# Kernel tuning notes

Hardware: AMD Instinct MI355X
Metric: run time of the kernel (lower is better)

The kernel has to match this reference:

```python
import jax, jax.numpy as jnp
import numpy as np

N_HEAD = 16

def setup_inputs() -> dict:
    key = jax.random.key(0)
    ks = jax.random.split(key, 5)
    B, S, D = 4, 2048, 1024
    return {
        "string": jax.random.normal(ks[0], (B, S, D), dtype=jnp.float32),
        "string_len": jax.random.randint(ks[1], (B,), 1, S + 1),
        "Wqkv": jax.random.normal(ks[2], (D, 3 * D), dtype=jnp.float32) * 0.02,
        "bqkv": jnp.zeros((3 * D,), dtype=jnp.float32),
        "Wo": jax.random.normal(ks[3], (D, D), dtype=jnp.float32) * 0.02,
        "bo": jnp.zeros((D,), dtype=jnp.float32),
    }


def reference(string, string_len, Wqkv, bqkv, Wo, bo):
    B, S, D = string.shape
    H = N_HEAD
    hd = D // H
    x = string @ Wqkv + bqkv                      # [B,S,3D]
    q, k, v = jnp.split(x, 3, axis=-1)
    # split heads -> [B,H,S,hd]
    q = q.reshape(B, S, H, hd).transpose(0, 2, 1, 3)
    k = k.reshape(B, S, H, hd).transpose(0, 2, 1, 3)
    v = v.reshape(B, S, H, hd).transpose(0, 2, 1, 3)
    w = jnp.einsum('bhqd,bhkd->bhqk', q, k) / jnp.sqrt(jnp.float32(hd))
    causal = jnp.tril(jnp.ones((S, S), dtype=bool))  # [S,S]
    w = jnp.where(causal[None, None], w, jnp.float32(-1e9))
    w = jax.nn.softmax(w, axis=-1)
    a = jnp.einsum('bhqk,bhkd->bhqd', w, v)       # [B,H,S,hd]
    a = a.transpose(0, 2, 1, 3).reshape(B, S, D)  # merge heads
    a = a @ Wo + bo
    return a, string_len
```

## Files before the change

kernel.cpp:

```cpp
#include <hip/hip_runtime.h>
#include <stdint.h>

typedef __attribute__((ext_vector_type(8))) short bf16x8;
typedef __attribute__((ext_vector_type(4))) float f32x4;
typedef __attribute__((ext_vector_type(16))) float f32x16;
typedef __attribute__((ext_vector_type(4))) unsigned short u16x4;

static constexpr int Bn = 4, Sn = 2048, Dn = 1024, Hn = 16, HD = 64;
static constexpr int Mrows = Bn * Sn;
static constexpr int D3 = 3 * Dn;

__device__ __forceinline__ unsigned short f2bf(float f) {
  unsigned int u = __float_as_uint(f);
  u += 0x7FFF + ((u >> 16) & 1);
  return (unsigned short)(u >> 16);
}

__device__ __forceinline__ void gload16(const void* gptr, void* lptr) {
  __builtin_amdgcn_global_load_lds(
      (__attribute__((address_space(1))) void*)gptr,
      (__attribute__((address_space(3))) void*)lptr, 16, 0, 0);
}

__device__ __forceinline__ int swz8(int r) { return (r ^ (r >> 3)) & 7; }

__device__ __forceinline__ float vexp2(float x) {
#if __has_builtin(__builtin_amdgcn_exp2f)
  return __builtin_amdgcn_exp2f(x);
#else
  return exp2f(x);
#endif
}

__device__ __forceinline__ unsigned cvtpk(float lo, float hi) {
  unsigned r;
  asm("v_cvt_pk_bf16_f32 %0, %1, %2" : "=v"(r) : "v"(lo), "v"(hi));
  return r;
}

__device__ __forceinline__ float lanepull(float v, int srclane) {
  return __int_as_float(__builtin_amdgcn_ds_bpermute(srclane * 4, __float_as_int(v)));
}

__global__ void cvt_f32_bf16(const float* __restrict__ in,
                             unsigned short* __restrict__ out, int n) {
  int i = (blockIdx.x * blockDim.x + threadIdx.x) * 4;
  if (i < n) {
    const float4 v = *(const float4*)(in + i);
    u16x4 o;
    o.x = f2bf(v.x); o.y = f2bf(v.y); o.z = f2bf(v.z); o.w = f2bf(v.w);
    *(u16x4*)(out + i) = o;
  }
}

__global__ void transpose_cvt(const float* __restrict__ W,
                              unsigned short* __restrict__ Wt, int K, int N) {
  __shared__ float tile[32][33];
  const int n0 = blockIdx.x * 32, k0 = blockIdx.y * 32;
  const int tx = threadIdx.x, ty = threadIdx.y;
  #pragma unroll
  for (int j = 0; j < 4; j++)
    tile[ty + 8 * j][tx] = W[(size_t)(k0 + ty + 8 * j) * N + n0 + tx];
  __syncthreads();
  #pragma unroll
  for (int j = 0; j < 4; j++)
    Wt[(size_t)(n0 + ty + 8 * j) * K + k0 + tx] = f2bf(tile[tx][ty + 8 * j]);
}

template<bool BF16_OUT>
__global__ __launch_bounds__(512, 1)
void gemm_bt2(const unsigned short* __restrict__ A,
              const unsigned short* __restrict__ Bt,
              const float* __restrict__ bias,
              void* __restrict__ Cout, int Nt, int Kt) {
  __shared__ __align__(128) unsigned char smem[98304];
  const int tid = threadIdx.x;
  const int w = tid >> 6, lane = tid & 63;
  const int wm = w >> 2, wn = w & 3;
  const int lrow = lane & 15, lk = lane >> 4;
  const long brow = (long)blockIdx.x * 128;
  const long bcol = (long)blockIdx.y * 256;

  const int srow = tid >> 3;
  const int sslot = tid & 7;

  auto stage = [&](int k0, unsigned char* buf) {
    unsigned char* Ab = buf;
    unsigned char* Bb = buf + 16384;
    #pragma unroll
    for (int i = 0; i < 2; i++) {
      const int r = srow + 64 * i;
      gload16(A + (size_t)(brow + r) * Kt + k0 + ((sslot ^ swz8(r)) * 8),
              Ab + w * 1024 + i * 8192);
    }
    #pragma unroll
    for (int i = 0; i < 4; i++) {
      const int r = srow + 64 * i;
      gload16(Bt + (size_t)(bcol + r) * Kt + k0 + ((sslot ^ swz8(r)) * 8),
              Bb + w * 1024 + i * 8192);
    }
  };

  f32x4 acc[4][4] = {};

  stage(0, smem);

  const int ntile = Kt >> 6;
  for (int t = 0; t < ntile; t++) {
    const int cur = t & 1;
    unsigned char* Ab = smem + cur * 49152;
    unsigned char* Bb = Ab + 16384;

    __builtin_amdgcn_s_barrier();
    if (t + 1 < ntile) {
      stage((t + 1) << 6, smem + (cur ^ 1) * 49152);
      asm volatile("s_waitcnt vmcnt(6)");
    } else {
      asm volatile("s_waitcnt vmcnt(0)");
    }
    __builtin_amdgcn_sched_barrier(0);
    __builtin_amdgcn_s_barrier();

    bf16x8 af[4][2], bfv[4][2];
    #pragma unroll
    for (int mt = 0; mt < 4; mt++) {
      const int r = wm * 64 + mt * 16 + lrow;
      #pragma unroll
      for (int kk = 0; kk < 2; kk++)
        af[mt][kk] = *(const bf16x8*)(Ab + r * 128 + (((kk * 4 + lk) ^ swz8(r)) * 16));
    }
    #pragma unroll
    for (int nt = 0; nt < 4; nt++) {
      const int r = wn * 64 + nt * 16 + lrow;
      #pragma unroll
      for (int kk = 0; kk < 2; kk++)
        bfv[nt][kk] = *(const bf16x8*)(Bb + r * 128 + (((kk * 4 + lk) ^ swz8(r)) * 16));
    }
    __builtin_amdgcn_s_setprio(1);
    #pragma unroll
    for (int mt = 0; mt < 4; mt++)
      #pragma unroll
      for (int nt = 0; nt < 4; nt++) {
        acc[mt][nt] = __builtin_amdgcn_mfma_f32_16x16x32_bf16(af[mt][0], bfv[nt][0], acc[mt][nt], 0, 0, 0);
        acc[mt][nt] = __builtin_amdgcn_mfma_f32_16x16x32_bf16(af[mt][1], bfv[nt][1], acc[mt][nt], 0, 0, 0);
      }
    __builtin_amdgcn_s_setprio(0);
  }

  #pragma unroll
  for (int nt = 0; nt < 4; nt++) {
    const long col = bcol + wn * 64 + nt * 16 + lrow;
    const float bv = bias[col];
    #pragma unroll
    for (int mt = 0; mt < 4; mt++) {
      #pragma unroll
      for (int rr = 0; rr < 4; rr++) {
        const long row = brow + wm * 64 + mt * 16 + lk * 4 + rr;
        const float v = acc[mt][nt][rr] + bv;
        if (BF16_OUT)
          ((unsigned short*)Cout)[row * Nt + col] = f2bf(v);
        else
          ((float*)Cout)[row * Nt + col] = v;
      }
    }
  }
}

__global__ __launch_bounds__(512, 2)
void attn_fwd2(const unsigned short* __restrict__ QKV,
               unsigned short* __restrict__ Out) {
  __shared__ __align__(128) unsigned char smem[65536];
  const int tid  = threadIdx.x;
  const int w    = tid >> 6;
  const int lane = tid & 63;
  const int li = lane & 31, hi = lane >> 5;
  const int bh = blockIdx.x;
  const int b  = bh >> 4, h = bh & 15;
  const int pb = blockIdx.y;
  const int qs = (w < 4) ? (63 - 4 * pb - w) : (4 * pb + (w - 4));
  const int wq = qs * 32;
  const int qrow = wq + li;

  bf16x8 qf[4];
  {
    const unsigned short* qp = QKV + (size_t)(b * Sn + qrow) * D3 + h * HD + hi * 8;
    #pragma unroll
    for (int ks = 0; ks < 4; ks++) qf[ks] = *(const bf16x8*)(qp + ks * 16);
  }

  f32x16 o0 = {}, o1 = {};
  float m = -3.0e38f, lsum = 0.f;
  const float cexp = 0.18033688011112042f;

  auto kstage = [&](int kb, unsigned char* Kb) {
    #pragma unroll
    for (int i = 0; i < 2; i++) {
      const int r    = w * 16 + i * 8 + (lane >> 3);
      const int slot = (lane & 7) ^ swz8(r);
      gload16(QKV + (size_t)(b * Sn + kb + r) * D3 + Dn + h * HD + slot * 8,
              Kb + w * 2048 + i * 1024);
    }
  };
  const int vkv8 = tid >> 3;
  const int vd0  = (tid & 7) * 8;
  auto vload = [&](int kb, int i) -> bf16x8 {
    return *(const bf16x8*)(QKV + (size_t)(b * Sn + kb + i * 64 + vkv8) * D3 + 2 * Dn + h * HD + vd0);
  };
  auto vwrite = [&](bf16x8 vv, int i, unsigned char* Vb) {
    const int kv = i * 64 + vkv8;
    #pragma unroll
    for (int j = 0; j < 8; j++) {
      const int d  = vd0 + j;
      const int vs = (d ^ (d >> 3)) & 15;
      *(unsigned short*)(Vb + d * 256 + (((kv >> 3) ^ vs) << 4) + (kv & 7) * 2) = (unsigned short)vv[j];
    }
  };

  auto substep = [&](int s, int kb, const unsigned char* Kb, const unsigned char* Vb) {
    f32x16 s0 = {}, s1 = {};
    const int r0 = s * 64 + li, r1 = s * 64 + 32 + li;
    __builtin_amdgcn_s_setprio(1);
    #pragma unroll
    for (int ks = 0; ks < 4; ks++) {
      const int slot = ks * 2 + hi;
      const bf16x8 k0 = *(const bf16x8*)(Kb + r0 * 128 + ((slot ^ swz8(r0)) * 16));
      const bf16x8 k1 = *(const bf16x8*)(Kb + r1 * 128 + ((slot ^ swz8(r1)) * 16));
      s0 = __builtin_amdgcn_mfma_f32_32x32x16_bf16(k0, qf[ks], s0, 0, 0, 0);
      s1 = __builtin_amdgcn_mfma_f32_32x32x16_bf16(k1, qf[ks], s1, 0, 0, 0);
    }
    __builtin_amdgcn_s_setprio(0);
    const int kbase = kb + s * 64;
    if (kbase + 63 > wq) {
      #pragma unroll
      for (int r = 0; r < 16; r++) {
        const int kvl = (r & 3) + 8 * (r >> 2) + 4 * hi;
        if (kbase + kvl > qrow)      s0[r] = -3.0e38f;
        if (kbase + 32 + kvl > qrow) s1[r] = -3.0e38f;
      }
    }
    float t8[8];
    #pragma unroll
    for (int r = 0; r < 8; r++)
      t8[r] = fmaxf(fmaxf(s0[r], s0[r + 8]), fmaxf(s1[r], s1[r + 8]));
    float tmax = fmaxf(fmaxf(fmaxf(t8[0], t8[1]), fmaxf(t8[2], t8[3])),
                       fmaxf(fmaxf(t8[4], t8[5]), fmaxf(t8[6], t8[7])));
    tmax = fmaxf(tmax, __shfl_xor(tmax, 32));
    if (__any(tmax > m + 44.0f)) {
      const float mn   = fmaxf(m, tmax);
      const float corr = vexp2((m - mn) * cexp);
      m = mn;
      lsum *= corr;
      #pragma unroll
      for (int r = 0; r < 16; r++) {
        const float cr = lanepull(corr, (r & 3) + 8 * (r >> 2) + 4 * hi);
        o0[r] *= cr; o1[r] *= cr;
      }
    }
    const float mc = m * cexp;
    f32x16 p0, p1;
    float psa = 0.f, psb = 0.f, psc = 0.f, psd = 0.f;
    #pragma unroll
    for (int r = 0; r < 16; r += 4) {
      p0[r] = vexp2(fmaf(s0[r], cexp, -mc));         psa += p0[r];
      p0[r + 1] = vexp2(fmaf(s0[r + 1], cexp, -mc)); psb += p0[r + 1];
      p0[r + 2] = vexp2(fmaf(s0[r + 2], cexp, -mc)); psc += p0[r + 2];
      p0[r + 3] = vexp2(fmaf(s0[r + 3], cexp, -mc)); psd += p0[r + 3];
    }
    #pragma unroll
    for (int r = 0; r < 16; r += 4) {
      p1[r] = vexp2(fmaf(s1[r], cexp, -mc));         psa += p1[r];
      p1[r + 1] = vexp2(fmaf(s1[r + 1], cexp, -mc)); psb += p1[r + 1];
      p1[r + 2] = vexp2(fmaf(s1[r + 2], cexp, -mc)); psc += p1[r + 2];
      p1[r + 3] = vexp2(fmaf(s1[r + 3], cexp, -mc)); psd += p1[r + 3];
    }
    lsum += (psa + psb) + (psc + psd);

    auto mk_pa = [&](const f32x16& pp, int base) -> bf16x8 {
      const unsigned a0 = cvtpk(pp[base + 0], pp[base + 1]);
      const unsigned a1 = cvtpk(pp[base + 2], pp[base + 3]);
      const unsigned b0 = cvtpk(pp[base + 4], pp[base + 5]);
      const unsigned b1 = cvtpk(pp[base + 6], pp[base + 7]);
      const unsigned xa0 = __shfl_xor(a0, 32), xa1 = __shfl_xor(a1, 32);
      const unsigned xb0 = __shfl_xor(b0, 32), xb1 = __shfl_xor(b1, 32);
      union { unsigned u[4]; bf16x8 v; } pu;
      pu.u[0] = hi ? xb0 : a0;
      pu.u[1] = hi ? xb1 : a1;
      pu.u[2] = hi ? b0  : xa0;
      pu.u[3] = hi ? b1  : xa1;
      return pu.v;
    };
    bf16x8 pa[4];
    pa[0] = mk_pa(p0, 0); pa[1] = mk_pa(p0, 8);
    pa[2] = mk_pa(p1, 0); pa[3] = mk_pa(p1, 8);

    const int vs0 = (li ^ (li >> 3)) & 15;
    const int vs1 = ((32 + li) ^ ((32 + li) >> 3)) & 15;
    __builtin_amdgcn_s_setprio(1);
    #pragma unroll
    for (int k16 = 0; k16 < 4; k16++) {
      const int slot = s * 8 + k16 * 2 + hi;
      const bf16x8 vb0 = *(const bf16x8*)(Vb + li * 256 + ((slot ^ vs0) << 4));
      const bf16x8 vb1 = *(const bf16x8*)(Vb + (32 + li) * 256 + ((slot ^ vs1) << 4));
      o0 = __builtin_amdgcn_mfma_f32_32x32x16_bf16(pa[k16], vb0, o0, 0, 0, 0);
      o1 = __builtin_amdgcn_mfma_f32_32x32x16_bf16(pa[k16], vb1, o1, 0, 0, 0);
    }
    __builtin_amdgcn_s_setprio(0);
  };

  kstage(0, smem);
  {
    bf16x8 va = vload(0, 0), vb = vload(0, 1);
    vwrite(va, 0, smem + 16384);
    vwrite(vb, 1, smem + 16384);
  }
  asm volatile("s_waitcnt lgkmcnt(0)");
  __builtin_amdgcn_sched_barrier(0);

  const int qsH = 63 - 4 * pb;
  const int nt  = ((qsH * 32 + 31) >> 7) + 1;
  for (int t = 0; t < nt; t++) {
    const int kb  = t << 7;
    const int cur = t & 1;
    unsigned char* Kb = smem + cur * 32768;
    unsigned char* Vb = Kb + 16384;
    const bool pre = (t + 1 < nt);
    bf16x8 vna, vnb;

    __builtin_amdgcn_s_barrier();
    if (pre) {
      kstage(kb + 128, smem + (cur ^ 1) * 32768);
      vna = vload(kb + 128, 0);
      vnb = vload(kb + 128, 1);
    }

    if (kb <= wq + 31) {
      substep(0, kb, Kb, Vb);
      if (kb + 64 <= wq + 31) substep(1, kb, Kb, Vb);
    }

    if (pre) {
      unsigned char* Vn = smem + (cur ^ 1) * 32768 + 16384;
      vwrite(vna, 0, Vn);
      vwrite(vnb, 1, Vn);
    }
    asm volatile("s_waitcnt lgkmcnt(0)");
    __builtin_amdgcn_sched_barrier(0);
  }

  const float lt = lsum + __shfl_xor(lsum, 32);
  const float rl = __builtin_amdgcn_rcpf(lt);
  #pragma unroll
  for (int r = 0; r < 16; r++) {
    const int q = (r & 3) + 8 * (r >> 2) + 4 * hi;
    const float rr = lanepull(rl, q);
    unsigned short* op = Out + (size_t)(b * Sn + wq + q) * Dn + h * HD;
    op[li]      = f2bf(o0[r] * rr);
    op[32 + li] = f2bf(o1[r] * rr);
  }
}

__global__ void copy_len(const int* __restrict__ slen, float* __restrict__ dst, int n) {
  const int i = threadIdx.x;
  if (i < n) dst[i] = (float)slen[i];
}

extern "C" void kernel_launch(void* const* d_in, const int* in_sizes, int n_in,
                              void* d_out, int out_size, void* d_ws, size_t ws_size,
                              hipStream_t stream) {
  const float* X    = (const float*)d_in[0];
  const int*   slen = (const int*)d_in[1];
  const float* Wqkv = (const float*)d_in[2];
  const float* bqkv = (const float*)d_in[3];
  const float* Wo   = (const float*)d_in[4];
  const float* bo   = (const float*)d_in[5];
  float* out = (float*)d_out;

  char* ws = (char*)d_ws;
  unsigned short* Xb    = (unsigned short*)ws;
  unsigned short* Wtq   = (unsigned short*)(ws + 16777216);
  unsigned short* Wto   = (unsigned short*)(ws + 16777216 + 6291456);
  unsigned short* QKVb  = (unsigned short*)(ws + 16777216 + 6291456 + 2097152);
  unsigned short* Attnb = Xb;

  cvt_f32_bf16<<<dim3(8192), dim3(256), 0, stream>>>(X, Xb, Mrows * Dn);
  transpose_cvt<<<dim3(96, 32), dim3(32, 8), 0, stream>>>(Wqkv, Wtq, Dn, D3);
  transpose_cvt<<<dim3(32, 32), dim3(32, 8), 0, stream>>>(Wo, Wto, Dn, Dn);

  gemm_bt2<true><<<dim3(64, 12), dim3(512), 0, stream>>>(Xb, Wtq, bqkv, (void*)QKVb, D3, Dn);
  attn_fwd2<<<dim3(64, 8), dim3(512), 0, stream>>>(QKVb, Attnb);
  gemm_bt2<false><<<dim3(64, 4), dim3(512), 0, stream>>>(Attnb, Wto, bo, d_out, Dn, Dn);
  copy_len<<<dim3(1), dim3(64), 0, stream>>>(slen, out + (size_t)Mrows * Dn, Bn);
}
```

Baseline: 188.5 us.

## Halve GEMM K-tile for two blocks per CU, remap grid, fix attention prefetch wait

The GEMM K-tile shrinks from 64 to 32, which halves shared memory to 48KB, and launch bounds now allow two 512-thread blocks per CU. The LDS swizzle moves to a 4-slot pattern to match the narrower rows. Block IDs are remapped across 8 groups (likely XCDs) through a 1D grid to improve L2 locality. The attention kernel now issues the V loads before the K stage and adds an explicit vmcnt wait plus a barrier before compute, trading an extra barrier per iteration for correct ordering of the prefetch. The smaller K-tile doubles the number of barriers per GEMM and halves the MFMA work between them.

Result: slower. 194.9 us (+3.4%).

```diff
diff --git a/kernel.cpp b/kernel.cpp
--- a/kernel.cpp
+++ b/kernel.cpp
@@ -23,6 +23,7 @@
 }
 
 __device__ __forceinline__ int swz8(int r) { return (r ^ (r >> 3)) & 7; }
+__device__ __forceinline__ int swz4(int r) { return (r ^ (r >> 2)) & 3; }
 
 __device__ __forceinline__ float vexp2(float x) {
 #if __has_builtin(__builtin_amdgcn_exp2f)
@@ -68,36 +69,35 @@
 }
 
 template<bool BF16_OUT>
-__global__ __launch_bounds__(512, 1)
-void gemm_bt2(const unsigned short* __restrict__ A,
+__global__ __launch_bounds__(512, 2)
+void gemm_bt3(const unsigned short* __restrict__ A,
               const unsigned short* __restrict__ Bt,
               const float* __restrict__ bias,
-              void* __restrict__ Cout, int Nt, int Kt) {
-  __shared__ __align__(128) unsigned char smem[98304];
+              void* __restrict__ Cout, int Nt, int Kt, int gx) {
+  __shared__ __align__(128) unsigned char smem[49152];
   const int tid = threadIdx.x;
   const int w = tid >> 6, lane = tid & 63;
   const int wm = w >> 2, wn = w & 3;
   const int lrow = lane & 15, lk = lane >> 4;
-  const long brow = (long)blockIdx.x * 128;
-  const long bcol = (long)blockIdx.y * 256;
-
-  const int srow = tid >> 3;
-  const int sslot = tid & 7;
+
+  const int n = gridDim.x;
+  const int id = blockIdx.x;
+  const int sid = (id & 7) * (n >> 3) + (id >> 3);
+  const long brow = (long)(sid % gx) * 128;
+  const long bcol = (long)(sid / gx) * 256;
+
+  const int srow = tid >> 2;
+  const int sslot = tid & 3;
 
   auto stage = [&](int k0, unsigned char* buf) {
-    unsigned char* Ab = buf;
-    unsigned char* Bb = buf + 16384;
+    gload16(A + (size_t)(brow + srow) * Kt + k0 + ((sslot ^ swz4(srow)) * 8),
+            buf + tid * 16);
+    unsigned char* Bb = buf + 8192;
     #pragma unroll
     for (int i = 0; i < 2; i++) {
-      const int r = srow + 64 * i;
-      gload16(A + (size_t)(brow + r) * Kt + k0 + ((sslot ^ swz8(r)) * 8),
-              Ab + w * 1024 + i * 8192);
-    }
-    #pragma unroll
-    for (int i = 0; i < 4; i++) {
-      const int r = srow + 64 * i;
-      gload16(Bt + (size_t)(bcol + r) * Kt + k0 + ((sslot ^ swz8(r)) * 8),
-              Bb + w * 1024 + i * 8192);
+      const int r = i * 128 + srow;
+      gload16(Bt + (size_t)(bcol + r) * Kt + k0 + ((sslot ^ swz4(r)) * 8),
+              Bb + i * 8192 + tid * 16);
     }
   };
 
@@ -105,45 +105,39 @@
 
   stage(0, smem);
 
-  const int ntile = Kt >> 6;
+  const int ntile = Kt >> 5;
   for (int t = 0; t < ntile; t++) {
     const int cur = t & 1;
-    unsigned char* Ab = smem + cur * 49152;
-    unsigned char* Bb = Ab + 16384;
+    unsigned char* Ab = smem + cur * 24576;
+    unsigned char* Bb = Ab + 8192;
 
     __builtin_amdgcn_s_barrier();
     if (t + 1 < ntile) {
-      stage((t + 1) << 6, smem + (cur ^ 1) * 49152);
-      asm volatile("s_waitcnt vmcnt(6)");
+      stage((t + 1) << 5, smem + (cur ^ 1) * 24576);
+      asm volatile("s_waitcnt vmcnt(3)");
     } else {
       asm volatile("s_waitcnt vmcnt(0)");
     }
     __builtin_amdgcn_sched_barrier(0);
     __builtin_amdgcn_s_barrier();
 
-    bf16x8 af[4][2], bfv[4][2];
+    bf16x8 af[4], bfv[4];
     #pragma unroll
     for (int mt = 0; mt < 4; mt++) {
       const int r = wm * 64 + mt * 16 + lrow;
-      #pragma unroll
-      for (int kk = 0; kk < 2; kk++)
-        af[mt][kk] = *(const bf16x8*)(Ab + r * 128 + (((kk * 4 + lk) ^ swz8(r)) * 16));
+      af[mt] = *(const bf16x8*)(Ab + r * 64 + ((lk ^ swz4(r)) * 16));
     }
     #pragma unroll
     for (int nt = 0; nt < 4; nt++) {
       const int r = wn * 64 + nt * 16 + lrow;
-      #pragma unroll
-      for (int kk = 0; kk < 2; kk++)
-        bfv[nt][kk] = *(const bf16x8*)(Bb + r * 128 + (((kk * 4 + lk) ^ swz8(r)) * 16));
+      bfv[nt] = *(const bf16x8*)(Bb + r * 64 + ((lk ^ swz4(r)) * 16));
     }
     __builtin_amdgcn_s_setprio(1);
     #pragma unroll
     for (int mt = 0; mt < 4; mt++)
       #pragma unroll
-      for (int nt = 0; nt < 4; nt++) {
-        acc[mt][nt] = __builtin_amdgcn_mfma_f32_16x16x32_bf16(af[mt][0], bfv[nt][0], acc[mt][nt], 0, 0, 0);
-        acc[mt][nt] = __builtin_amdgcn_mfma_f32_16x16x32_bf16(af[mt][1], bfv[nt][1], acc[mt][nt], 0, 0, 0);
-      }
+      for (int nt = 0; nt < 4; nt++)
+        acc[mt][nt] = __builtin_amdgcn_mfma_f32_16x16x32_bf16(af[mt], bfv[nt], acc[mt][nt], 0, 0, 0);
     __builtin_amdgcn_s_setprio(0);
   }
 
@@ -328,10 +322,15 @@
 
     __builtin_amdgcn_s_barrier();
     if (pre) {
-      kstage(kb + 128, smem + (cur ^ 1) * 32768);
       vna = vload(kb + 128, 0);
       vnb = vload(kb + 128, 1);
-    }
+      kstage(kb + 128, smem + (cur ^ 1) * 32768);
+      asm volatile("s_waitcnt vmcnt(4)");
+    } else {
+      asm volatile("s_waitcnt vmcnt(0)");
+    }
+    __builtin_amdgcn_sched_barrier(0);
+    __builtin_amdgcn_s_barrier();
 
     if (kb <= wq + 31) {
       substep(0, kb, Kb, Vb);
@@ -386,8 +385,8 @@
   transpose_cvt<<<dim3(96, 32), dim3(32, 8), 0, stream>>>(Wqkv, Wtq, Dn, D3);
   transpose_cvt<<<dim3(32, 32), dim3(32, 8), 0, stream>>>(Wo, Wto, Dn, Dn);
 
-  gemm_bt2<true><<<dim3(64, 12), dim3(512), 0, stream>>>(Xb, Wtq, bqkv, (void*)QKVb, D3, Dn);
+  gemm_bt3<true><<<dim3(768), dim3(512), 0, stream>>>(Xb, Wtq, bqkv, (void*)QKVb, D3, Dn, 64);
   attn_fwd2<<<dim3(64, 8), dim3(512), 0, stream>>>(QKVb, Attnb);
-  gemm_bt2<false><<<dim3(64, 4), dim3(512), 0, stream>>>(Attnb, Wto, bo, d_out, Dn, Dn);
+  gemm_bt3<false><<<dim3(256), dim3(512), 0, stream>>>(Attnb, Wto, bo, d_out, Dn, Dn, 64);
   copy_len<<<dim3(1), dim3(64), 0, stream>>>(slen, out + (size_t)Mrows * Dn, Bn);
 }
```
